# Optimization experiments

Hardware: AMD Instinct MI355X
Metric: run time of the kernel (lower is better)

## Reference

```python
import jax, jax.numpy as jnp
import numpy as np

N, NFEAT, NHID, NCLASS, NHEADS = 4096, 256, 16, 16, 8
ALPHA = 0.2
NEG_INF = -9e15


def setup_inputs() -> dict:
    key = jax.random.key(0)
    ks = jax.random.split(key, 8)
    x = jax.random.normal(ks[0], (N, NFEAT), dtype=jnp.float32)
    adj = (jax.random.uniform(ks[1], (N, N)) < 0.01).astype(jnp.float32)
    adj = jnp.maximum(adj, jnp.eye(N, dtype=jnp.float32))
    # per-head weights for the NHEADS concat layers
    W = jax.random.normal(ks[2], (NHEADS, NFEAT, NHID), dtype=jnp.float32) * 0.1
    a_src = jax.random.normal(ks[3], (NHEADS, NHID), dtype=jnp.float32) * 0.1
    a_dst = jax.random.normal(ks[4], (NHEADS, NHID), dtype=jnp.float32) * 0.1
    # output attention layer (concat=False)
    W_out = jax.random.normal(ks[5], (NHEADS * NHID, NCLASS), dtype=jnp.float32) * 0.1
    a_out_src = jax.random.normal(ks[6], (NCLASS,), dtype=jnp.float32) * 0.1
    a_out_dst = jax.random.normal(ks[7], (NCLASS,), dtype=jnp.float32) * 0.1
    return {"x": x, "adj": adj, "W": W, "a_src": a_src, "a_dst": a_dst,
            "W_out": W_out, "a_out_src": a_out_src, "a_out_dst": a_out_dst}


def _gat_layer(h, adj_mask, W, a_s, a_d, concat):
    # h: [N,F]; W: [H,F,D] (or [F,D] for single head treated as H=1)
    Wh = jnp.einsum('nf,hfd->hnd', h, W)              # [H,N,D]
    src = jnp.einsum('hnd,hd->hn', Wh, a_s)           # [H,N]
    dst = jnp.einsum('hnd,hd->hn', Wh, a_d)           # [H,N]
    e = jax.nn.leaky_relu(src[:, :, None] + dst[:, None, :], ALPHA)  # [H,N,N]
    e = jnp.where(adj_mask > 0, e, NEG_INF)
    att = jax.nn.softmax(e, axis=-1)                  # masked softmax over neighbors
    out = jnp.einsum('hnm,hmd->hnd', att, Wh)         # [H,N,D]
    if concat:
        out = jax.nn.elu(out)
    return out


def reference(x, adj, W, a_src, a_dst, W_out, a_out_src, a_out_dst):
    # multi-head concat layers (dropout in eval mode -> identity)
    h = _gat_layer(x, adj, W, a_src, a_dst, concat=True)          # [H,N,D]
    h = jnp.transpose(h, (1, 0, 2)).reshape(N, NHEADS * NHID)     # concat heads
    # output attention layer (single head, concat=False), then outer ELU
    out = _gat_layer(h, adj, W_out[None], a_out_src[None], a_out_dst[None], concat=False)
    return jax.nn.elu(out[0])                                     # [N, NCLASS]
```

## Files before the change

### kernel.cpp

```cpp
#include <hip/hip_runtime.h>

#define NN 4096
#define NFEAT 256
#define NHID 16
#define NHEADS 8
#define NCLASS 16
#define MAXN 256
#define LALPHA 0.2f

__global__ void build_nbr_kernel(const float* __restrict__ adj,
                                 int* __restrict__ nbr, int* __restrict__ cnt) {
  int row = blockIdx.x;
  const float4* arow = reinterpret_cast<const float4*>(adj + (size_t)row * NN);
  __shared__ int scnt;
  if (threadIdx.x == 0) scnt = 0;
  __syncthreads();
  int* rn = nbr + (size_t)row * MAXN;
#pragma unroll
  for (int it = 0; it < NN / 4 / 256; ++it) {
    int q = threadIdx.x + it * 256;
    float4 v = arow[q];
    int base = q * 4;
    if (v.x > 0.f) { int p = atomicAdd(&scnt, 1); if (p < MAXN) rn[p] = base + 0; }
    if (v.y > 0.f) { int p = atomicAdd(&scnt, 1); if (p < MAXN) rn[p] = base + 1; }
    if (v.z > 0.f) { int p = atomicAdd(&scnt, 1); if (p < MAXN) rn[p] = base + 2; }
    if (v.w > 0.f) { int p = atomicAdd(&scnt, 1); if (p < MAXN) rn[p] = base + 3; }
  }
  __syncthreads();
  if (threadIdx.x == 0) cnt[row] = scnt < MAXN ? scnt : MAXN;
}

__global__ void layer1_proj_kernel(const float* __restrict__ x,
                                   const float* __restrict__ W,
                                   const float* __restrict__ a_src,
                                   const float* __restrict__ a_dst,
                                   float* __restrict__ Wh1,
                                   float* __restrict__ src1,
                                   float* __restrict__ dst1) {
  int n = blockIdx.x;
  int t = threadIdx.x;
  __shared__ float xs[NFEAT];
  reinterpret_cast<float2*>(xs)[t] =
      reinterpret_cast<const float2*>(x + (size_t)n * NFEAT)[t];
  __syncthreads();
  int h = t >> 4, d = t & 15;
  const float* Wp = W + h * (NFEAT * NHID) + d;
  float acc = 0.f;
#pragma unroll 16
  for (int f = 0; f < NFEAT; ++f) acc += xs[f] * Wp[f * NHID];
  Wh1[(size_t)n * (NHEADS * NHID) + t] = acc;
  float vs = acc * a_src[h * NHID + d];
  float vd = acc * a_dst[h * NHID + d];
#pragma unroll
  for (int off = 8; off >= 1; off >>= 1) {
    vs += __shfl_xor(vs, off);
    vd += __shfl_xor(vd, off);
  }
  if (d == 0) {
    src1[n * NHEADS + h] = vs;
    dst1[n * NHEADS + h] = vd;
  }
}

__global__ void layer1_agg_kernel(const int* __restrict__ nbr, const int* __restrict__ cnt,
                                  const float* __restrict__ Wh1,
                                  const float* __restrict__ src1, const float* __restrict__ dst1,
                                  const float* __restrict__ Wout,
                                  const float* __restrict__ a2s, const float* __restrict__ a2d,
                                  float* __restrict__ Wh2, float* __restrict__ src2,
                                  float* __restrict__ dst2) {
  int n = blockIdx.x;
  int t = threadIdx.x;
  int h = t >> 4;
  int c = cnt[n];
  const int* nb = nbr + (size_t)n * MAXN;
  __shared__ float e[MAXN * NHEADS];
  __shared__ float mh[NHEADS], rs[NHEADS];
  __shared__ float hs[NHEADS * NHID];
  for (int idx = t; idx < c * NHEADS; idx += 128) {
    int j = idx >> 3, hh = idx & 7;
    float ee = src1[n * NHEADS + hh] + dst1[nb[j] * NHEADS + hh];
    ee = ee > 0.f ? ee : LALPHA * ee;
    e[idx] = ee;
  }
  __syncthreads();
  if (t < NHEADS) {
    float m = -1e30f;
    for (int j = 0; j < c; ++j) m = fmaxf(m, e[j * NHEADS + t]);
    float s = 0.f;
    for (int j = 0; j < c; ++j) s += expf(e[j * NHEADS + t] - m);
    mh[t] = m;
    rs[t] = 1.f / s;
  }
  __syncthreads();
  for (int idx = t; idx < c * NHEADS; idx += 128) {
    int hh = idx & 7;
    e[idx] = expf(e[idx] - mh[hh]) * rs[hh];
  }
  __syncthreads();
  float acc = 0.f;
  for (int j = 0; j < c; ++j)
    acc += e[j * NHEADS + h] * Wh1[(size_t)nb[j] * (NHEADS * NHID) + t];
  float hv = acc > 0.f ? acc : (expf(acc) - 1.f);
  hs[t] = hv;
  __syncthreads();
  if (t < NCLASS) {
    float a = 0.f;
#pragma unroll 16
    for (int k = 0; k < NHEADS * NHID; ++k) a += hs[k] * Wout[k * NCLASS + t];
    Wh2[n * NCLASS + t] = a;
    float vs = a * a2s[t];
    float vd = a * a2d[t];
#pragma unroll
    for (int off = 8; off >= 1; off >>= 1) {
      vs += __shfl_xor(vs, off);
      vd += __shfl_xor(vd, off);
    }
    if (t == 0) {
      src2[n] = vs;
      dst2[n] = vd;
    }
  }
}

__global__ void layer2_agg_kernel(const int* __restrict__ nbr, const int* __restrict__ cnt,
                                  const float* __restrict__ Wh2,
                                  const float* __restrict__ src2, const float* __restrict__ dst2,
                                  float* __restrict__ out) {
  int g = threadIdx.x >> 4, d = threadIdx.x & 15;
  int n = blockIdx.x * 16 + g;
  int c = cnt[n];
  const int* nb = nbr + (size_t)n * MAXN;
  float si = src2[n];
  float m = -1e30f;
  for (int j = 0; j < c; ++j) {
    float ee = si + dst2[nb[j]];
    ee = ee > 0.f ? ee : LALPHA * ee;
    m = fmaxf(m, ee);
  }
  float s = 0.f, acc = 0.f;
  for (int j = 0; j < c; ++j) {
    int jj = nb[j];
    float ee = si + dst2[jj];
    ee = ee > 0.f ? ee : LALPHA * ee;
    float w = expf(ee - m);
    s += w;
    acc += w * Wh2[jj * NCLASS + d];
  }
  acc /= s;
  out[n * NCLASS + d] = acc > 0.f ? acc : (expf(acc) - 1.f);
}

extern "C" void kernel_launch(void* const* d_in, const int* in_sizes, int n_in,
                              void* d_out, int out_size, void* d_ws, size_t ws_size,
                              hipStream_t stream) {
  const float* x     = (const float*)d_in[0];
  const float* adj   = (const float*)d_in[1];
  const float* W     = (const float*)d_in[2];
  const float* a_src = (const float*)d_in[3];
  const float* a_dst = (const float*)d_in[4];
  const float* W_out = (const float*)d_in[5];
  const float* a_os  = (const float*)d_in[6];
  const float* a_od  = (const float*)d_in[7];
  float* out = (float*)d_out;

  char* ws = (char*)d_ws;
  size_t off = 0;
  auto alloc = [&](size_t bytes) -> void* {
    void* p = ws + off;
    off += (bytes + 255) & ~(size_t)255;
    return p;
  };
  int*   nbr  = (int*)alloc((size_t)NN * MAXN * sizeof(int));
  int*   cnt  = (int*)alloc((size_t)NN * sizeof(int));
  float* Wh1  = (float*)alloc((size_t)NN * NHEADS * NHID * sizeof(float));
  float* src1 = (float*)alloc((size_t)NN * NHEADS * sizeof(float));
  float* dst1 = (float*)alloc((size_t)NN * NHEADS * sizeof(float));
  float* Wh2  = (float*)alloc((size_t)NN * NCLASS * sizeof(float));
  float* src2 = (float*)alloc((size_t)NN * sizeof(float));
  float* dst2 = (float*)alloc((size_t)NN * sizeof(float));

  hipLaunchKernelGGL(build_nbr_kernel, dim3(NN), dim3(256), 0, stream, adj, nbr, cnt);
  hipLaunchKernelGGL(layer1_proj_kernel, dim3(NN), dim3(128), 0, stream,
                     x, W, a_src, a_dst, Wh1, src1, dst1);
  hipLaunchKernelGGL(layer1_agg_kernel, dim3(NN), dim3(128), 0, stream,
                     nbr, cnt, Wh1, src1, dst1, W_out, a_os, a_od, Wh2, src2, dst2);
  hipLaunchKernelGGL(layer2_agg_kernel, dim3(NN / 16), dim3(256), 0, stream,
                     nbr, cnt, Wh2, src2, dst2, out);
}
```

Baseline: 171.3 us.

## Merge neighbor build and projection kernels, use wave ballots and parallel softmax

Combines adjacency compaction and the layer-1 projection into a single launch by splitting the grid. Neighbor compaction now uses per-wave ballots with one shared atomic per wave instead of one per element. The projection tiles 16 nodes per block with register blocking. Layer-1 aggregation caches neighbor indices in shared memory, stores scores head-major, runs the softmax with 16 lanes per head instead of one thread, and splits the output projection across threads. Fast exp intrinsics and unroll pragmas are added, which slightly changes numerics. Note that neighbor order within a row is no longer sorted.

```diff
diff --git a/kernel.cpp b/kernel.cpp
--- a/kernel.cpp
+++ b/kernel.cpp
@@ -4,151 +4,184 @@
 #define NFEAT 256
 #define NHID 16
 #define NHEADS 8
+#define NCOL 128
 #define NCLASS 16
 #define MAXN 256
 #define LALPHA 0.2f
-
-__global__ void build_nbr_kernel(const float* __restrict__ adj,
-                                 int* __restrict__ nbr, int* __restrict__ cnt) {
-  int row = blockIdx.x;
-  const float4* arow = reinterpret_cast<const float4*>(adj + (size_t)row * NN);
+#define BNODES 16
+#define XPAD 20
+#define EPAD 260
+
+__global__ __launch_bounds__(256) void prep_kernel(
+    const float* __restrict__ adj, const float* __restrict__ x,
+    const float* __restrict__ W, const float* __restrict__ a_src,
+    const float* __restrict__ a_dst,
+    int* __restrict__ nbr, int* __restrict__ cnt,
+    float* __restrict__ Wh1, float* __restrict__ src1, float* __restrict__ dst1) {
+  __shared__ float xT[NFEAT * XPAD];
   __shared__ int scnt;
-  if (threadIdx.x == 0) scnt = 0;
-  __syncthreads();
-  int* rn = nbr + (size_t)row * MAXN;
-#pragma unroll
-  for (int it = 0; it < NN / 4 / 256; ++it) {
-    int q = threadIdx.x + it * 256;
-    float4 v = arow[q];
-    int base = q * 4;
-    if (v.x > 0.f) { int p = atomicAdd(&scnt, 1); if (p < MAXN) rn[p] = base + 0; }
-    if (v.y > 0.f) { int p = atomicAdd(&scnt, 1); if (p < MAXN) rn[p] = base + 1; }
-    if (v.z > 0.f) { int p = atomicAdd(&scnt, 1); if (p < MAXN) rn[p] = base + 2; }
-    if (v.w > 0.f) { int p = atomicAdd(&scnt, 1); if (p < MAXN) rn[p] = base + 3; }
-  }
-  __syncthreads();
-  if (threadIdx.x == 0) cnt[row] = scnt < MAXN ? scnt : MAXN;
-}
-
-__global__ void layer1_proj_kernel(const float* __restrict__ x,
-                                   const float* __restrict__ W,
-                                   const float* __restrict__ a_src,
-                                   const float* __restrict__ a_dst,
-                                   float* __restrict__ Wh1,
-                                   float* __restrict__ src1,
-                                   float* __restrict__ dst1) {
-  int n = blockIdx.x;
   int t = threadIdx.x;
-  __shared__ float xs[NFEAT];
-  reinterpret_cast<float2*>(xs)[t] =
-      reinterpret_cast<const float2*>(x + (size_t)n * NFEAT)[t];
-  __syncthreads();
-  int h = t >> 4, d = t & 15;
-  const float* Wp = W + h * (NFEAT * NHID) + d;
-  float acc = 0.f;
-#pragma unroll 16
-  for (int f = 0; f < NFEAT; ++f) acc += xs[f] * Wp[f * NHID];
-  Wh1[(size_t)n * (NHEADS * NHID) + t] = acc;
-  float vs = acc * a_src[h * NHID + d];
-  float vd = acc * a_dst[h * NHID + d];
-#pragma unroll
-  for (int off = 8; off >= 1; off >>= 1) {
-    vs += __shfl_xor(vs, off);
-    vd += __shfl_xor(vd, off);
-  }
-  if (d == 0) {
-    src1[n * NHEADS + h] = vs;
-    dst1[n * NHEADS + h] = vd;
-  }
-}
-
-__global__ void layer1_agg_kernel(const int* __restrict__ nbr, const int* __restrict__ cnt,
-                                  const float* __restrict__ Wh1,
-                                  const float* __restrict__ src1, const float* __restrict__ dst1,
-                                  const float* __restrict__ Wout,
-                                  const float* __restrict__ a2s, const float* __restrict__ a2d,
-                                  float* __restrict__ Wh2, float* __restrict__ src2,
-                                  float* __restrict__ dst2) {
-  int n = blockIdx.x;
-  int t = threadIdx.x;
-  int h = t >> 4;
+
+  if (blockIdx.x < NN) {
+    int row = blockIdx.x;
+    const float4* arow = reinterpret_cast<const float4*>(adj + (size_t)row * NN);
+    if (t == 0) scnt = 0;
+    __syncthreads();
+    int* rn = nbr + (size_t)row * MAXN;
+    int lane = t & 63;
+    unsigned long long below = lane ? (~0ULL >> (64 - lane)) : 0ULL;
+#pragma unroll
+    for (int it = 0; it < NN / 4 / 256; ++it) {
+      int q = t + it * 256;
+      float4 v = arow[q];
+      int base = q * 4;
+      unsigned long long m0 = __ballot(v.x > 0.f);
+      unsigned long long m1 = __ballot(v.y > 0.f);
+      unsigned long long m2 = __ballot(v.z > 0.f);
+      unsigned long long m3 = __ballot(v.w > 0.f);
+      int c0 = __popcll(m0), c1 = __popcll(m1), c2 = __popcll(m2), c3 = __popcll(m3);
+      int tot = c0 + c1 + c2 + c3;
+      int wbase = 0;
+      if (lane == 0 && tot) wbase = atomicAdd(&scnt, tot);
+      wbase = __shfl(wbase, 0);
+      if (v.x > 0.f) { int p = wbase + __popcll(m0 & below);           if (p < MAXN) rn[p] = base;     }
+      if (v.y > 0.f) { int p = wbase + c0 + __popcll(m1 & below);      if (p < MAXN) rn[p] = base + 1; }
+      if (v.z > 0.f) { int p = wbase + c0 + c1 + __popcll(m2 & below); if (p < MAXN) rn[p] = base + 2; }
+      if (v.w > 0.f) { int p = wbase + c0 + c1 + c2 + __popcll(m3 & below); if (p < MAXN) rn[p] = base + 3; }
+    }
+    __syncthreads();
+    if (t == 0) cnt[row] = scnt < MAXN ? scnt : MAXN;
+  } else {
+    int bn = (blockIdx.x - NN) * BNODES;
+#pragma unroll
+    for (int it = 0; it < BNODES; ++it) {
+      xT[t * XPAD + it] = x[(size_t)(bn + it) * NFEAT + t];
+    }
+    __syncthreads();
+    int cg = t & 31, ng = t >> 5;
+    const float* Wp = W + (cg >> 2) * (NFEAT * NHID) + ((cg & 3) << 2);
+    float acc[2][4] = {};
+#pragma unroll 4
+    for (int f = 0; f < NFEAT; ++f) {
+      float4 wv = *reinterpret_cast<const float4*>(Wp + f * NHID);
+      float2 xv = *reinterpret_cast<const float2*>(&xT[f * XPAD + ng * 2]);
+      acc[0][0] += xv.x * wv.x; acc[0][1] += xv.x * wv.y;
+      acc[0][2] += xv.x * wv.z; acc[0][3] += xv.x * wv.w;
+      acc[1][0] += xv.y * wv.x; acc[1][1] += xv.y * wv.y;
+      acc[1][2] += xv.y * wv.z; acc[1][3] += xv.y * wv.w;
+    }
+    int col0 = cg * 4;
+    float4 as4 = *reinterpret_cast<const float4*>(a_src + col0);
+    float4 ad4 = *reinterpret_cast<const float4*>(a_dst + col0);
+#pragma unroll
+    for (int i = 0; i < 2; ++i) {
+      int n = bn + ng * 2 + i;
+      *reinterpret_cast<float4*>(Wh1 + (size_t)n * NCOL + col0) =
+          make_float4(acc[i][0], acc[i][1], acc[i][2], acc[i][3]);
+      float vs = acc[i][0] * as4.x + acc[i][1] * as4.y + acc[i][2] * as4.z + acc[i][3] * as4.w;
+      float vd = acc[i][0] * ad4.x + acc[i][1] * ad4.y + acc[i][2] * ad4.z + acc[i][3] * ad4.w;
+      vs += __shfl_xor(vs, 1); vs += __shfl_xor(vs, 2);
+      vd += __shfl_xor(vd, 1); vd += __shfl_xor(vd, 2);
+      if ((cg & 3) == 0) {
+        src1[n * NHEADS + (cg >> 2)] = vs;
+        dst1[n * NHEADS + (cg >> 2)] = vd;
+      }
+    }
+  }
+}
+
+__global__ __launch_bounds__(128) void layer1_agg_kernel(
+    const int* __restrict__ nbr, const int* __restrict__ cnt,
+    const float* __restrict__ Wh1, const float* __restrict__ src1,
+    const float* __restrict__ dst1, const float* __restrict__ Wout,
+    const float* __restrict__ a2s, const float* __restrict__ a2d,
+    float* __restrict__ Wh2, float* __restrict__ src2, float* __restrict__ dst2) {
+  int n = blockIdx.x, t = threadIdx.x;
+  int h = t >> 4, l = t & 15;
   int c = cnt[n];
-  const int* nb = nbr + (size_t)n * MAXN;
-  __shared__ float e[MAXN * NHEADS];
-  __shared__ float mh[NHEADS], rs[NHEADS];
-  __shared__ float hs[NHEADS * NHID];
+  __shared__ int snb[MAXN];
+  __shared__ float e[NHEADS * EPAD];
+  __shared__ float hs[NCOL];
+  __shared__ float part[NHEADS][NCLASS];
+  for (int j = t; j < c; j += 128) snb[j] = nbr[(size_t)n * MAXN + j];
+  __syncthreads();
   for (int idx = t; idx < c * NHEADS; idx += 128) {
     int j = idx >> 3, hh = idx & 7;
-    float ee = src1[n * NHEADS + hh] + dst1[nb[j] * NHEADS + hh];
-    ee = ee > 0.f ? ee : LALPHA * ee;
-    e[idx] = ee;
-  }
-  __syncthreads();
-  if (t < NHEADS) {
-    float m = -1e30f;
-    for (int j = 0; j < c; ++j) m = fmaxf(m, e[j * NHEADS + t]);
-    float s = 0.f;
-    for (int j = 0; j < c; ++j) s += expf(e[j * NHEADS + t] - m);
-    mh[t] = m;
-    rs[t] = 1.f / s;
-  }
-  __syncthreads();
-  for (int idx = t; idx < c * NHEADS; idx += 128) {
-    int hh = idx & 7;
-    e[idx] = expf(e[idx] - mh[hh]) * rs[hh];
-  }
+    float ee = src1[n * NHEADS + hh] + dst1[snb[j] * NHEADS + hh];
+    e[hh * EPAD + j] = ee > 0.f ? ee : LALPHA * ee;
+  }
+  __syncthreads();
+  float m = -1e30f;
+  for (int j = l; j < c; j += 16) m = fmaxf(m, e[h * EPAD + j]);
+  m = fmaxf(m, __shfl_xor(m, 8)); m = fmaxf(m, __shfl_xor(m, 4));
+  m = fmaxf(m, __shfl_xor(m, 2)); m = fmaxf(m, __shfl_xor(m, 1));
+  float s = 0.f;
+  for (int j = l; j < c; j += 16) {
+    float w = __expf(e[h * EPAD + j] - m);
+    e[h * EPAD + j] = w;
+    s += w;
+  }
+  s += __shfl_xor(s, 8); s += __shfl_xor(s, 4);
+  s += __shfl_xor(s, 2); s += __shfl_xor(s, 1);
+  float rs = 1.f / s;
   __syncthreads();
   float acc = 0.f;
+#pragma unroll 4
   for (int j = 0; j < c; ++j)
-    acc += e[j * NHEADS + h] * Wh1[(size_t)nb[j] * (NHEADS * NHID) + t];
-  float hv = acc > 0.f ? acc : (expf(acc) - 1.f);
-  hs[t] = hv;
+    acc += e[h * EPAD + j] * Wh1[(size_t)snb[j] * NCOL + t];
+  acc *= rs;
+  hs[t] = acc > 0.f ? acc : (__expf(acc) - 1.f);
+  __syncthreads();
+  int cc = t & 15, kg = t >> 4;
+  float p = 0.f;
+#pragma unroll
+  for (int k = 0; k < 16; ++k)
+    p += hs[kg * 16 + k] * Wout[(kg * 16 + k) * NCLASS + cc];
+  part[kg][cc] = p;
   __syncthreads();
   if (t < NCLASS) {
     float a = 0.f;
-#pragma unroll 16
-    for (int k = 0; k < NHEADS * NHID; ++k) a += hs[k] * Wout[k * NCLASS + t];
+#pragma unroll
+    for (int kg2 = 0; kg2 < NHEADS; ++kg2) a += part[kg2][t];
     Wh2[n * NCLASS + t] = a;
-    float vs = a * a2s[t];
-    float vd = a * a2d[t];
+    float vs = a * a2s[t], vd = a * a2d[t];
 #pragma unroll
     for (int off = 8; off >= 1; off >>= 1) {
       vs += __shfl_xor(vs, off);
       vd += __shfl_xor(vd, off);
     }
-    if (t == 0) {
-      src2[n] = vs;
-      dst2[n] = vd;
-    }
-  }
-}
-
-__global__ void layer2_agg_kernel(const int* __restrict__ nbr, const int* __restrict__ cnt,
-                                  const float* __restrict__ Wh2,
-                                  const float* __restrict__ src2, const float* __restrict__ dst2,
-                                  float* __restrict__ out) {
+    if (t == 0) { src2[n] = vs; dst2[n] = vd; }
+  }
+}
+
+__global__ __launch_bounds__(256) void layer2_agg_kernel(
+    const int* __restrict__ nbr, const int* __restrict__ cnt,
+    const float* __restrict__ Wh2, const float* __restrict__ src2,
+    const float* __restrict__ dst2, float* __restrict__ out) {
   int g = threadIdx.x >> 4, d = threadIdx.x & 15;
   int n = blockIdx.x * 16 + g;
   int c = cnt[n];
   const int* nb = nbr + (size_t)n * MAXN;
   float si = src2[n];
   float m = -1e30f;
+#pragma unroll 4
   for (int j = 0; j < c; ++j) {
     float ee = si + dst2[nb[j]];
     ee = ee > 0.f ? ee : LALPHA * ee;
     m = fmaxf(m, ee);
   }
   float s = 0.f, acc = 0.f;
+#pragma unroll 2
   for (int j = 0; j < c; ++j) {
     int jj = nb[j];
     float ee = si + dst2[jj];
     ee = ee > 0.f ? ee : LALPHA * ee;
-    float w = expf(ee - m);
+    float w = __expf(ee - m);
     s += w;
     acc += w * Wh2[jj * NCLASS + d];
   }
   acc /= s;
-  out[n * NCLASS + d] = acc > 0.f ? acc : (expf(acc) - 1.f);
+  out[n * NCLASS + d] = acc > 0.f ? acc : (__expf(acc) - 1.f);
 }
 
 extern "C" void kernel_launch(void* const* d_in, const int* in_sizes, int n_in,
@@ -173,16 +206,15 @@
   };
   int*   nbr  = (int*)alloc((size_t)NN * MAXN * sizeof(int));
   int*   cnt  = (int*)alloc((size_t)NN * sizeof(int));
-  float* Wh1  = (float*)alloc((size_t)NN * NHEADS * NHID * sizeof(float));
+  float* Wh1  = (float*)alloc((size_t)NN * NCOL * sizeof(float));
   float* src1 = (float*)alloc((size_t)NN * NHEADS * sizeof(float));
   float* dst1 = (float*)alloc((size_t)NN * NHEADS * sizeof(float));
   float* Wh2  = (float*)alloc((size_t)NN * NCLASS * sizeof(float));
   float* src2 = (float*)alloc((size_t)NN * sizeof(float));
   float* dst2 = (float*)alloc((size_t)NN * sizeof(float));
 
-  hipLaunchKernelGGL(build_nbr_kernel, dim3(NN), dim3(256), 0, stream, adj, nbr, cnt);
-  hipLaunchKernelGGL(layer1_proj_kernel, dim3(NN), dim3(128), 0, stream,
-                     x, W, a_src, a_dst, Wh1, src1, dst1);
+  hipLaunchKernelGGL(prep_kernel, dim3(NN + NN / BNODES), dim3(256), 0, stream,
+                     adj, x, W, a_src, a_dst, nbr, cnt, Wh1, src1, dst1);
   hipLaunchKernelGGL(layer1_agg_kernel, dim3(NN), dim3(128), 0, stream,
                      nbr, cnt, Wh1, src1, dst1, W_out, a_os, a_od, Wh2, src2, dst2);
   hipLaunchKernelGGL(layer2_agg_kernel, dim3(NN / 16), dim3(256), 0, stream,
```

Result: faster. 165.5 us (-3.4%).
